# Performance work log

Measured on AMD Instinct MI355X. Metric: run time of the kernel, lower is better.

Reference implementation:

```python
import jax, jax.numpy as jnp
import numpy as np

HIDDEN = 2048
N_HEADS = 16
N_KV_HEADS = 4
HEAD_DIM = HIDDEN // N_HEADS  # 128
ROPE_THETA = 10000.0


def setup_inputs() -> dict:
    key = jax.random.key(0)
    ks = jax.random.split(key, 5)
    B, S = 2, 2048
    scale = 0.02
    return {
        "hidden_states": jax.random.normal(ks[0], (B, S, HIDDEN), jnp.float32),
        "Wq": jax.random.normal(ks[1], (HIDDEN, N_HEADS * HEAD_DIM), jnp.float32) * scale,
        "Wk": jax.random.normal(ks[2], (HIDDEN, N_KV_HEADS * HEAD_DIM), jnp.float32) * scale,
        "Wv": jax.random.normal(ks[3], (HIDDEN, N_KV_HEADS * HEAD_DIM), jnp.float32) * scale,
        "Wo": jax.random.normal(ks[4], (HIDDEN, HIDDEN), jnp.float32) * scale,
    }


def _rope_tables(seq_len, dim, dtype):
    inv_freq = 1.0 / (ROPE_THETA ** (jnp.arange(0, dim, 2, dtype=jnp.float32) / dim))
    t = jnp.arange(seq_len, dtype=jnp.float32)
    freqs = jnp.outer(t, inv_freq)            # [S, dim/2]
    emb = jnp.concatenate([freqs, freqs], -1)  # [S, dim]
    return jnp.cos(emb).astype(dtype), jnp.sin(emb).astype(dtype)


def _rotate_half(x):
    d = x.shape[-1] // 2
    return jnp.concatenate([-x[..., d:], x[..., :d]], axis=-1)


def _mqa_forward(hidden_states, Wq, Wk, Wv, Wo):
    B, S, _ = hidden_states.shape
    q = (hidden_states @ Wq).reshape(B, S, N_HEADS, HEAD_DIM).transpose(0, 2, 1, 3)      # [B,H,S,D]
    k = (hidden_states @ Wk).reshape(B, S, N_KV_HEADS, HEAD_DIM).transpose(0, 2, 1, 3)   # [B,Hkv,S,D]
    v = (hidden_states @ Wv).reshape(B, S, N_KV_HEADS, HEAD_DIM).transpose(0, 2, 1, 3)

    cos, sin = _rope_tables(S, HEAD_DIM, q.dtype)  # [S,D]
    q = q * cos + _rotate_half(q) * sin
    k = k * cos + _rotate_half(k) * sin

    # GQA: group query heads over shared KV heads instead of repeat_kv (same math)
    g = N_HEADS // N_KV_HEADS
    qg = q.reshape(B, N_KV_HEADS, g, S, HEAD_DIM)
    scale = 1.0 / np.sqrt(HEAD_DIM)
    scores = jnp.einsum("bhgqd,bhkd->bhgqk", qg, k) * scale  # [B,Hkv,g,S,S]
    causal = jnp.tril(jnp.ones((S, S), bool))
    scores = jnp.where(causal, scores, -jnp.inf)
    probs = jax.nn.softmax(scores.astype(jnp.float32), axis=-1).astype(q.dtype)
    out = jnp.einsum("bhgqk,bhkd->bhgqd", probs, v)  # [B,Hkv,g,S,D]
    out = out.reshape(B, N_HEADS, S, HEAD_DIM).transpose(0, 2, 1, 3).reshape(B, S, HIDDEN)
    return out @ Wo


def reference(hidden_states, Wq, Wk, Wv, Wo):
    return _mqa_forward(hidden_states, Wq, Wk, Wv, Wo)
```

## Files before the change

### kernel.cpp

```cpp
#include <hip/hip_runtime.h>
#include <hip/hip_bf16.h>
#include <cstdint>
#include <cstddef>

#define HIDDEN   2048
#define NH       16
#define NKV      4
#define HD       128
#define SEQ      2048
#define BATCH    2
#define NTOK     (BATCH*SEQ)
#define QKV_LD   3072
#define KOFF     2048
#define VOFF     2560
#define SM_SCALE 0.08838834764831845f
#define LOG2E    1.4426950408889634f

typedef __attribute__((ext_vector_type(8)))  short bf16x8;
typedef __attribute__((ext_vector_type(4)))  float f32x4v;
typedef __attribute__((ext_vector_type(16))) float f32x16;
typedef unsigned short ushort_t;

__device__ __forceinline__ unsigned short f2bf(float f) {
  return __builtin_bit_cast(unsigned short, __float2bfloat16(f));
}
__device__ __forceinline__ float bf2f(ushort_t u) {
  return __builtin_bit_cast(float, (unsigned)u << 16);
}
__device__ __forceinline__ unsigned pack2(float a, float b) {
  return (unsigned)f2bf(a) | ((unsigned)f2bf(b) << 16);
}

__device__ __forceinline__ void gload16(const void* g, void* l) {
  __builtin_amdgcn_global_load_lds(
      (const __attribute__((address_space(1))) unsigned int*)g,
      (__attribute__((address_space(3))) unsigned int*)l, 16, 0, 0);
}

__global__ __launch_bounds__(256) void conv_f2b(
    const float* __restrict__ in, ushort_t* __restrict__ out, int n8)
{
  const int i = blockIdx.x*256 + threadIdx.x;
  if (i >= n8) return;
  const float4 a = ((const float4*)in)[2*i];
  const float4 b = ((const float4*)in)[2*i + 1];
  uint4 r;
  r.x = pack2(a.x, a.y); r.y = pack2(a.z, a.w);
  r.z = pack2(b.x, b.y); r.w = pack2(b.z, b.w);
  ((uint4*)out)[i] = r;
}

__global__ __launch_bounds__(256) void transpose_f2b(
    const float* __restrict__ W, ushort_t* __restrict__ Wt, int K, int N)
{
  __shared__ float tile[32][33];
  const int n0 = blockIdx.x*32, k0 = blockIdx.y*32;
  const int tx = threadIdx.x & 31, ty = threadIdx.x >> 5;
  #pragma unroll
  for (int i = 0; i < 4; ++i)
    tile[ty*4 + i][tx] = W[(size_t)(k0 + ty*4 + i)*N + n0 + tx];
  __syncthreads();
  #pragma unroll
  for (int i = 0; i < 4; ++i) {
    const int nl = ty*4 + i;
    Wt[(size_t)(n0 + nl)*K + k0 + tx] = f2bf(tile[tx][nl]);
  }
}

template<bool B16OUT>
__global__ __launch_bounds__(256) void bt_gemm(
    const ushort_t* __restrict__ A, const ushort_t* __restrict__ Bt,
    void* __restrict__ Cv, int ldc)
{
  __shared__ ushort_t As[128*64];
  __shared__ ushort_t Bs[128*64];
  const int t = threadIdx.x, lane = t & 63, w = t >> 6;
  const int bm = blockIdx.y*128, bn = blockIdx.x*128;
  const int wr = w >> 1, wc = w & 1;
  const int lr = lane & 15, lg = lane >> 4;

  f32x4v acc[4][4];
  #pragma unroll
  for (int fm = 0; fm < 4; ++fm)
    #pragma unroll
    for (int fn = 0; fn < 4; ++fn)
      #pragma unroll
      for (int r = 0; r < 4; ++r) acc[fm][fn][r] = 0.f;

  const char* Ab = (const char*)A;
  const char* Bb = (const char*)Bt;
  char* asb = (char*)As;
  char* bsb = (char*)Bs;

  for (int kt = 0; kt < HIDDEN*2; kt += 128) {
    __syncthreads();
    #pragma unroll
    for (int u = 0; u < 4; ++u) {
      const int idx = u*256 + t;
      const int row = idx >> 3;
      const int kb  = (idx & 7) * 16;
      const int skb = kb ^ ((row & 7) << 4);
      gload16(Ab + (size_t)(bm + row)*4096 + kt + skb, asb + idx*16);
      gload16(Bb + (size_t)(bn + row)*4096 + kt + skb, bsb + idx*16);
    }
    __syncthreads();
    #pragma unroll
    for (int kc = 0; kc < 2; ++kc) {
      bf16x8 af[4], bfr[4];
      #pragma unroll
      for (int f = 0; f < 4; ++f) {
        const int rm = wr*64 + f*16 + lr;
        af[f]  = *(const bf16x8*)(asb + rm*128 + ((kc*64 + lg*16) ^ ((rm & 7) << 4)));
        const int rn = wc*64 + f*16 + lr;
        bfr[f] = *(const bf16x8*)(bsb + rn*128 + ((kc*64 + lg*16) ^ ((rn & 7) << 4)));
      }
      #pragma unroll
      for (int fm = 0; fm < 4; ++fm)
        #pragma unroll
        for (int fn = 0; fn < 4; ++fn)
          acc[fm][fn] = __builtin_amdgcn_mfma_f32_16x16x32_bf16(af[fm], bfr[fn], acc[fm][fn], 0, 0, 0);
    }
  }

  #pragma unroll
  for (int fm = 0; fm < 4; ++fm) {
    const int m = bm + wr*64 + fm*16 + lg*4;
    #pragma unroll
    for (int fn = 0; fn < 4; ++fn) {
      const int n = bn + wc*64 + fn*16 + lr;
      #pragma unroll
      for (int r = 0; r < 4; ++r) {
        if constexpr (B16OUT)
          ((ushort_t*)Cv)[(size_t)(m + r)*ldc + n] = f2bf(acc[fm][fn][r]);
        else
          ((float*)Cv)[(size_t)(m + r)*ldc + n] = acc[fm][fn][r];
      }
    }
  }
}

__global__ __launch_bounds__(256) void rope_conv(
    const ushort_t* __restrict__ QKVb, ushort_t* __restrict__ Qo,
    ushort_t* __restrict__ Ko)
{
  const int total = NTOK * (NH + NKV) * (HD/2);
  int idx = blockIdx.x * 256 + threadIdx.x;
  if (idx >= total) return;
  const int i   = idx & 63;
  int tmp = idx >> 6;
  const int hs  = tmp % (NH + NKV);
  const int tkn = tmp / (NH + NKV);
  const int s   = tkn & (SEQ - 1);
  const int b   = tkn >> 11;
  const float invf = expf(-(float)i * 0.14391156831212787f);
  float sn, cs;
  sincosf((float)s * invf, &sn, &cs);
  const size_t base = (size_t)tkn * QKV_LD + (hs < NH ? hs * HD : KOFF + (hs - NH) * HD);
  const float x0 = bf2f(QKVb[base + i]);
  const float x1 = bf2f(QKVb[base + i + 64]);
  const float y0 = x0 * cs - x1 * sn;
  const float y1 = x1 * cs + x0 * sn;
  if (hs < NH) {
    ushort_t* q = Qo + (size_t)tkn * HIDDEN + hs * HD;
    q[i]      = f2bf(y0 * (SM_SCALE * LOG2E));
    q[i + 64] = f2bf(y1 * (SM_SCALE * LOG2E));
  } else {
    ushort_t* k = Ko + ((size_t)(b*NKV + (hs - NH))*SEQ + s) * HD;
    k[i]      = f2bf(y0);
    k[i + 64] = f2bf(y1);
  }
}

__global__ __launch_bounds__(256) void vt_conv(
    const ushort_t* __restrict__ QKVb, ushort_t* __restrict__ Vtb)
{
  __shared__ ushort_t tile[32][33];
  const int s0 = blockIdx.x*32;
  const int d0 = (blockIdx.y & 3)*32;
  const int bk = blockIdx.y >> 2;
  const int b = bk >> 2, hk = bk & 3;
  const int tx = threadIdx.x & 31, ty = threadIdx.x >> 5;
  #pragma unroll
  for (int i = 0; i < 4; ++i) {
    const int sl = ty*4 + i;
    tile[sl][tx] = QKVb[(size_t)(b*SEQ + s0 + sl)*QKV_LD + VOFF + hk*HD + d0 + tx];
  }
  __syncthreads();
  #pragma unroll
  for (int i = 0; i < 4; ++i) {
    const int dl = ty*4 + i;
    Vtb[((size_t)bk*HD + d0 + dl)*SEQ + s0 + tx] = tile[tx][dl];
  }
}

__global__ __launch_bounds__(128) void attn_mfma4(
    const ushort_t* __restrict__ Qb, const ushort_t* __restrict__ Kb,
    const ushort_t* __restrict__ Vtb, ushort_t* __restrict__ O)
{
  __shared__ ushort_t Kl[64*128];
  __shared__ ushort_t Vl[128*64];
  __shared__ ushort_t Pl[2][32*64];

  const int bh = blockIdx.x;
  const int qb = 31 - blockIdx.y;
  const int b = bh >> 4, h = bh & 15, hk = h >> 2;
  const int t = threadIdx.x, w = t >> 6, lane = t & 63;
  const int c = lane & 31, hi = lane >> 5;
  const int qw0 = qb*64 + w*32;
  const int qg  = qw0 + c;

  const char* Kbb = (const char*)(Kb + (size_t)(b*NKV + hk)*SEQ*HD);
  const char* Vbb = (const char*)(Vtb + (size_t)(b*NKV + hk)*HD*SEQ);
  char* plb = (char*)Pl[w];
  char* klds = (char*)Kl;
  char* vlds = (char*)Vl;

  int ksrc[8], vsrc[8], ldst[8];
  #pragma unroll
  for (int u = 0; u < 8; ++u) {
    const int idx = u*128 + t;
    const int krow = idx >> 4, kof = (idx & 15) << 4;
    ksrc[u] = krow*256 + (kof ^ ((krow & 15) << 4));
    const int vd = idx >> 3,  vof = (idx & 7) << 4;
    vsrc[u] = vd*(SEQ*2) + (vof ^ ((vd & 7) << 4));
    ldst[u] = idx*16;
  }

  bf16x8 qf[8];
  {
    const ushort_t* qrow = Qb + (size_t)(b*SEQ + qg)*HIDDEN + h*HD;
    #pragma unroll
    for (int kc = 0; kc < 8; ++kc)
      qf[kc] = *(const bf16x8*)(qrow + kc*16 + hi*8);
  }

  f32x16 ot[4];
  #pragma unroll
  for (int nc = 0; nc < 4; ++nc)
    #pragma unroll
    for (int r = 0; r < 16; ++r) ot[nc][r] = 0.f;
  float m = -1e30f, l = 0.f;

  #pragma unroll
  for (int u = 0; u < 8; ++u) {
    gload16(Kbb + ksrc[u], klds + ldst[u]);
    gload16(Vbb + vsrc[u], vlds + ldst[u]);
  }
  __syncthreads();

  for (int kt = 0; kt <= qb; ++kt) {
    f32x16 s[2];
    #pragma unroll
    for (int kn = 0; kn < 2; ++kn)
      #pragma unroll
      for (int r = 0; r < 16; ++r) s[kn][r] = 0.f;
    #pragma unroll
    for (int kn = 0; kn < 2; ++kn) {
      const int row = kn*32 + c;
      const int sw = (row & 15) << 4;
      #pragma unroll
      for (int kc = 0; kc < 8; ++kc) {
        const bf16x8 ka = *(const bf16x8*)(klds + row*256 + ((kc*32 + hi*16) ^ sw));
        s[kn] = __builtin_amdgcn_mfma_f32_32x32x16_bf16(ka, qf[kc], s[kn], 0, 0, 0);
      }
    }
    if (kt == qb) {
      #pragma unroll
      for (int kn = 0; kn < 2; ++kn)
        #pragma unroll
        for (int r = 0; r < 16; ++r) {
          const int kg_ = kt*64 + kn*32 + (r & 3) + 8*(r >> 2) + 4*hi;
          if (kg_ > qg) s[kn][r] = -1e30f;
        }
    }
    float mx[16];
    #pragma unroll
    for (int r = 0; r < 16; ++r) mx[r] = fmaxf(s[0][r], s[1][r]);
    #pragma unroll
    for (int st = 8; st > 0; st >>= 1)
      #pragma unroll
      for (int r = 0; r < 8; ++r)
        if (r < st) mx[r] = fmaxf(mx[r], mx[r + st]);
    const float pm = fmaxf(mx[0], __shfl_xor(mx[0], 32));
    if (!__all(pm - m <= 8.f)) {
      const float mnew = fmaxf(m, pm);
      const float corr = exp2f(m - mnew);
      m = mnew;
      l *= corr;
      #pragma unroll
      for (int nc = 0; nc < 4; ++nc) ot[nc] *= corr;
    }
    float ls = 0.f;
    #pragma unroll
    for (int kn = 0; kn < 2; ++kn)
      #pragma unroll
      for (int r = 0; r < 16; ++r) {
        const float p = exp2f(s[kn][r] - m);
        ls += p;
        s[kn][r] = p;
      }
    l += ls;
    {
      const int swp = (c & 7) << 4;
      #pragma unroll
      for (int kn = 0; kn < 2; ++kn)
        #pragma unroll
        for (int r = 0; r < 16; r += 2) {
          const int key = kn*32 + (r & 3) + 8*(r >> 2) + 4*hi;
          *(unsigned*)(plb + c*128 + ((key*2) ^ swp)) = pack2(s[kn][r], s[kn][r+1]);
        }
    }
    asm volatile("s_waitcnt lgkmcnt(0)" ::: "memory");
    #pragma unroll
    for (int kc = 0; kc < 4; ++kc) {
      const bf16x8 pb = *(const bf16x8*)(plb + c*128 + ((kc*32 + hi*16) ^ ((c & 7) << 4)));
      #pragma unroll
      for (int nc = 0; nc < 4; ++nc) {
        const int dim = nc*32 + c;
        const bf16x8 va = *(const bf16x8*)(vlds + dim*128 + ((kc*32 + hi*16) ^ ((dim & 7) << 4)));
        ot[nc] = __builtin_amdgcn_mfma_f32_32x32x16_bf16(va, pb, ot[nc], 0, 0, 0);
      }
    }
    if (kt < qb) {
      __syncthreads();
      const size_t kto = (size_t)(kt + 1) * 16384;
      const int    vto = (kt + 1) * 128;
      #pragma unroll
      for (int u = 0; u < 8; ++u) {
        gload16(Kbb + kto + ksrc[u], klds + ldst[u]);
        gload16(Vbb + vto + vsrc[u], vlds + ldst[u]);
      }
      __syncthreads();
    }
  }

  const float lt = l + __shfl_xor(l, 32);
  const float inv = 1.f / lt;
  ushort_t* orow = O + (size_t)(b*SEQ + qg) * HIDDEN + h*HD;
  #pragma unroll
  for (int nc = 0; nc < 4; ++nc)
    #pragma unroll
    for (int r = 0; r < 16; r += 2) {
      const int dim = nc*32 + (r & 3) + 8*(r >> 2) + 4*hi;
      *(unsigned*)(orow + dim) = pack2(ot[nc][r]*inv, ot[nc][r+1]*inv);
    }
}

extern "C" void kernel_launch(void* const* d_in, const int* in_sizes, int n_in,
                              void* d_out, int out_size, void* d_ws, size_t ws_size,
                              hipStream_t stream)
{
  (void)in_sizes; (void)n_in; (void)out_size; (void)ws_size;
  const float* H  = (const float*)d_in[0];
  const float* Wq = (const float*)d_in[1];
  const float* Wk = (const float*)d_in[2];
  const float* Wv = (const float*)d_in[3];
  const float* Wo = (const float*)d_in[4];
  float* out = (float*)d_out;

  char* ws = (char*)d_ws;
  ushort_t* QKVb = (ushort_t*)ws;
  ushort_t* Hb   = (ushort_t*)(ws + 25165824);
  ushort_t* Qb   = Hb;
  ushort_t* Wt   = (ushort_t*)(ws + 41943040);
  ushort_t* Kb   = (ushort_t*)(ws + 54525952);
  ushort_t* Vtb  = (ushort_t*)(ws + 58720256);
  ushort_t* Oat  = (ushort_t*)(ws + 62914560);

  conv_f2b<<<4096, 256, 0, stream>>>(H, Hb, NTOK*HIDDEN/8);
  transpose_f2b<<<dim3(64, 64), 256, 0, stream>>>(Wq, Wt,                     2048, 2048);
  transpose_f2b<<<dim3(16, 64), 256, 0, stream>>>(Wk, Wt + (size_t)2048*2048, 2048, 512);
  transpose_f2b<<<dim3(16, 64), 256, 0, stream>>>(Wv, Wt + (size_t)2560*2048, 2048, 512);

  bt_gemm<true><<<dim3(QKV_LD/128, NTOK/128), 256, 0, stream>>>(Hb, Wt, QKVb, QKV_LD);

  const int rope_total = NTOK * (NH + NKV) * (HD/2);
  rope_conv<<<(rope_total + 255)/256, 256, 0, stream>>>(QKVb, Qb, Kb);
  vt_conv<<<dim3(SEQ/32, 32), 256, 0, stream>>>(QKVb, Vtb);

  attn_mfma4<<<dim3(32, 32), 128, 0, stream>>>(Qb, Kb, Vtb, Oat);

  transpose_f2b<<<dim3(64, 64), 256, 0, stream>>>(Wo, Wt, 2048, 2048);
  bt_gemm<false><<<dim3(HIDDEN/128, NTOK/128), 256, 0, stream>>>(Oat, Wt, out, HIDDEN);
}
```

Baseline: 244.2 us.

## Split attention KV range across four waves per 32-query tile with LDS merge

The attention kernel changes from two waves each owning 32 queries over a 64-key tile to four waves sharing one 32-query tile. Each wave handles a different 32-key slice of a 128-key K/V tile, and the per-wave softmax states are merged at the end through shared memory. This doubles the grid and uses larger K/V tiles, aiming for more parallelism and fewer barriers per key. The cost is 80KB of LDS per block, which limits occupancy, plus an extra reduction pass and idle waves on the diagonal tiles.

```diff
diff --git a/kernel.cpp b/kernel.cpp
--- a/kernel.cpp
+++ b/kernel.cpp
@@ -193,37 +193,32 @@
   }
 }
 
-__global__ __launch_bounds__(128) void attn_mfma4(
+__global__ __launch_bounds__(256) void attn_mfma5(
     const ushort_t* __restrict__ Qb, const ushort_t* __restrict__ Kb,
     const ushort_t* __restrict__ Vtb, ushort_t* __restrict__ O)
 {
-  __shared__ ushort_t Kl[64*128];
-  __shared__ ushort_t Vl[128*64];
-  __shared__ ushort_t Pl[2][32*64];
+  __shared__ char smem[81920];
 
   const int bh = blockIdx.x;
-  const int qb = 31 - blockIdx.y;
+  const int qt = 63 - (int)blockIdx.y;
   const int b = bh >> 4, h = bh & 15, hk = h >> 2;
   const int t = threadIdx.x, w = t >> 6, lane = t & 63;
   const int c = lane & 31, hi = lane >> 5;
-  const int qw0 = qb*64 + w*32;
+  const int qw0 = qt*32;
   const int qg  = qw0 + c;
+  const int nsteps = (qt + 4) >> 2;
 
   const char* Kbb = (const char*)(Kb + (size_t)(b*NKV + hk)*SEQ*HD);
   const char* Vbb = (const char*)(Vtb + (size_t)(b*NKV + hk)*HD*SEQ);
-  char* plb = (char*)Pl[w];
-  char* klds = (char*)Kl;
-  char* vlds = (char*)Vl;
-
-  int ksrc[8], vsrc[8], ldst[8];
+  char* plb = smem + 65536 + w*4096;
+
+  int ksrc[8], vsrc[8];
   #pragma unroll
   for (int u = 0; u < 8; ++u) {
-    const int idx = u*128 + t;
-    const int krow = idx >> 4, kof = (idx & 15) << 4;
-    ksrc[u] = krow*256 + (kof ^ ((krow & 15) << 4));
-    const int vd = idx >> 3,  vof = (idx & 7) << 4;
-    vsrc[u] = vd*(SEQ*2) + (vof ^ ((vd & 7) << 4));
-    ldst[u] = idx*16;
+    const int idx = u*256 + t;
+    const int row = idx >> 4, of = (idx & 15) << 4;
+    ksrc[u] = row*256 + (of ^ ((row & 15) << 4));
+    vsrc[u] = row*(SEQ*2) + (of ^ ((row & 15) << 4));
   }
 
   bf16x8 qf[8];
@@ -239,111 +234,137 @@
   for (int nc = 0; nc < 4; ++nc)
     #pragma unroll
     for (int r = 0; r < 16; ++r) ot[nc][r] = 0.f;
-  float m = -1e30f, l = 0.f;
+  float m = -3000.f, l = 0.f;
 
   #pragma unroll
   for (int u = 0; u < 8; ++u) {
-    gload16(Kbb + ksrc[u], klds + ldst[u]);
-    gload16(Vbb + vsrc[u], vlds + ldst[u]);
+    const int idx = u*256 + t;
+    gload16(Kbb + ksrc[u], smem + idx*16);
+    gload16(Vbb + vsrc[u], smem + 32768 + idx*16);
   }
   __syncthreads();
 
-  for (int kt = 0; kt <= qb; ++kt) {
-    f32x16 s[2];
-    #pragma unroll
-    for (int kn = 0; kn < 2; ++kn)
-      #pragma unroll
-      for (int r = 0; r < 16; ++r) s[kn][r] = 0.f;
-    #pragma unroll
-    for (int kn = 0; kn < 2; ++kn) {
-      const int row = kn*32 + c;
-      const int sw = (row & 15) << 4;
-      #pragma unroll
-      for (int kc = 0; kc < 8; ++kc) {
-        const bf16x8 ka = *(const bf16x8*)(klds + row*256 + ((kc*32 + hi*16) ^ sw));
-        s[kn] = __builtin_amdgcn_mfma_f32_32x32x16_bf16(ka, qf[kc], s[kn], 0, 0, 0);
-      }
-    }
-    if (kt == qb) {
-      #pragma unroll
-      for (int kn = 0; kn < 2; ++kn)
+  for (int ktp = 0; ktp < nsteps; ++ktp) {
+    const bool skip = (ktp*128 + w*32) > (qw0 + 31);
+    if (!skip) {
+      f32x16 s;
+      #pragma unroll
+      for (int r = 0; r < 16; ++r) s[r] = 0.f;
+      {
+        const int key = w*32 + c;
+        const int sw = (key & 15) << 4;
+        const char* krow = smem + key*256;
+        #pragma unroll
+        for (int kc = 0; kc < 8; ++kc) {
+          const bf16x8 ka = *(const bf16x8*)(krow + ((kc*32 + hi*16) ^ sw));
+          s = __builtin_amdgcn_mfma_f32_32x32x16_bf16(ka, qf[kc], s, 0, 0, 0);
+        }
+      }
+      if (ktp*128 + 127 > qw0) {
         #pragma unroll
         for (int r = 0; r < 16; ++r) {
-          const int kg_ = kt*64 + kn*32 + (r & 3) + 8*(r >> 2) + 4*hi;
-          if (kg_ > qg) s[kn][r] = -1e30f;
+          const int kg_ = ktp*128 + w*32 + (r & 3) + 8*(r >> 2) + 4*hi;
+          if (kg_ > qg) s[r] = -30000.f;
         }
-    }
-    float mx[16];
-    #pragma unroll
-    for (int r = 0; r < 16; ++r) mx[r] = fmaxf(s[0][r], s[1][r]);
-    #pragma unroll
-    for (int st = 8; st > 0; st >>= 1)
-      #pragma unroll
-      for (int r = 0; r < 8; ++r)
-        if (r < st) mx[r] = fmaxf(mx[r], mx[r + st]);
-    const float pm = fmaxf(mx[0], __shfl_xor(mx[0], 32));
-    if (!__all(pm - m <= 8.f)) {
-      const float mnew = fmaxf(m, pm);
-      const float corr = exp2f(m - mnew);
-      m = mnew;
-      l *= corr;
-      #pragma unroll
-      for (int nc = 0; nc < 4; ++nc) ot[nc] *= corr;
-    }
-    float ls = 0.f;
-    #pragma unroll
-    for (int kn = 0; kn < 2; ++kn)
+      }
+      float mx[8];
+      #pragma unroll
+      for (int r = 0; r < 8; ++r) mx[r] = fmaxf(s[r], s[r + 8]);
+      #pragma unroll
+      for (int st = 4; st > 0; st >>= 1)
+        #pragma unroll
+        for (int r = 0; r < 4; ++r)
+          if (r < st) mx[r] = fmaxf(mx[r], mx[r + st]);
+      const float pm = fmaxf(mx[0], __shfl_xor(mx[0], 32));
+      if (!__all(pm - m <= 8.f)) {
+        const float mnew = fmaxf(m, pm);
+        const float corr = exp2f(m - mnew);
+        m = mnew;
+        l *= corr;
+        #pragma unroll
+        for (int nc = 0; nc < 4; ++nc) ot[nc] *= corr;
+      }
+      float ls = 0.f;
       #pragma unroll
       for (int r = 0; r < 16; ++r) {
-        const float p = exp2f(s[kn][r] - m);
+        const float p = exp2f(s[r] - m);
         ls += p;
-        s[kn][r] = p;
-      }
-    l += ls;
-    {
-      const int swp = (c & 7) << 4;
-      #pragma unroll
-      for (int kn = 0; kn < 2; ++kn)
+        s[r] = p;
+      }
+      l += ls;
+      {
+        const int swp = (c & 7) << 4;
         #pragma unroll
         for (int r = 0; r < 16; r += 2) {
-          const int key = kn*32 + (r & 3) + 8*(r >> 2) + 4*hi;
-          *(unsigned*)(plb + c*128 + ((key*2) ^ swp)) = pack2(s[kn][r], s[kn][r+1]);
+          const int kl_ = (r & 3) + 8*(r >> 2) + 4*hi;
+          *(unsigned*)(plb + c*128 + ((kl_*2) ^ swp)) = pack2(s[r], s[r+1]);
         }
-    }
-    asm volatile("s_waitcnt lgkmcnt(0)" ::: "memory");
-    #pragma unroll
-    for (int kc = 0; kc < 4; ++kc) {
-      const bf16x8 pb = *(const bf16x8*)(plb + c*128 + ((kc*32 + hi*16) ^ ((c & 7) << 4)));
-      #pragma unroll
-      for (int nc = 0; nc < 4; ++nc) {
-        const int dim = nc*32 + c;
-        const bf16x8 va = *(const bf16x8*)(vlds + dim*128 + ((kc*32 + hi*16) ^ ((dim & 7) << 4)));
-        ot[nc] = __builtin_amdgcn_mfma_f32_32x32x16_bf16(va, pb, ot[nc], 0, 0, 0);
-      }
-    }
-    if (kt < qb) {
+      }
+      asm volatile("s_waitcnt lgkmcnt(0)" ::: "memory");
+      #pragma unroll
+      for (int kcl = 0; kcl < 2; ++kcl) {
+        const bf16x8 pb = *(const bf16x8*)(plb + c*128 + ((kcl*32 + hi*16) ^ ((c & 7) << 4)));
+        #pragma unroll
+        for (int nc = 0; nc < 4; ++nc) {
+          const int dim = nc*32 + c;
+          const bf16x8 va = *(const bf16x8*)(smem + 32768 + dim*256 +
+              ((w*64 + kcl*32 + hi*16) ^ ((dim & 15) << 4)));
+          ot[nc] = __builtin_amdgcn_mfma_f32_32x32x16_bf16(va, pb, ot[nc], 0, 0, 0);
+        }
+      }
+    }
+    if (ktp < nsteps - 1) {
       __syncthreads();
-      const size_t kto = (size_t)(kt + 1) * 16384;
-      const int    vto = (kt + 1) * 128;
+      const size_t kto = (size_t)(ktp + 1) * 32768;
+      const int    vto = (ktp + 1) * 256;
       #pragma unroll
       for (int u = 0; u < 8; ++u) {
-        gload16(Kbb + kto + ksrc[u], klds + ldst[u]);
-        gload16(Vbb + vto + vsrc[u], vlds + ldst[u]);
+        const int idx = u*256 + t;
+        gload16(Kbb + kto + ksrc[u], smem + idx*16);
+        gload16(Vbb + vto + vsrc[u], smem + 32768 + idx*16);
       }
       __syncthreads();
     }
   }
 
-  const float lt = l + __shfl_xor(l, 32);
-  const float inv = 1.f / lt;
-  ushort_t* orow = O + (size_t)(b*SEQ + qg) * HIDDEN + h*HD;
-  #pragma unroll
-  for (int nc = 0; nc < 4; ++nc)
-    #pragma unroll
-    for (int r = 0; r < 16; r += 2) {
-      const int dim = nc*32 + (r & 3) + 8*(r >> 2) + 4*hi;
-      *(unsigned*)(orow + dim) = pack2(ot[nc][r]*inv, ot[nc][r+1]*inv);
-    }
+  __syncthreads();
+  float* ob = (float*)smem;
+  if (w > 0) {
+    float* dst = ob + ((w - 1)*64 + lane)*66;
+    #pragma unroll
+    for (int nc = 0; nc < 4; ++nc)
+      #pragma unroll
+      for (int r = 0; r < 16; ++r) dst[nc*16 + r] = ot[nc][r];
+    dst[64] = m;
+    dst[65] = l;
+  }
+  __syncthreads();
+  if (w == 0) {
+    #pragma unroll 1
+    for (int wi = 0; wi < 3; ++wi) {
+      const float* src = ob + (wi*64 + lane)*66;
+      const float mw = src[64], lw = src[65];
+      const float mn = fmaxf(m, mw);
+      const float c0 = exp2f(m - mn), c1 = exp2f(mw - mn);
+      m = mn;
+      l = l*c0 + lw*c1;
+      #pragma unroll
+      for (int nc = 0; nc < 4; ++nc)
+        #pragma unroll
+        for (int r = 0; r < 16; ++r)
+          ot[nc][r] = ot[nc][r]*c0 + src[nc*16 + r]*c1;
+    }
+    const float lt = l + __shfl_xor(l, 32);
+    const float inv = 1.f / lt;
+    ushort_t* orow = O + (size_t)(b*SEQ + qg) * HIDDEN + h*HD;
+    #pragma unroll
+    for (int nc = 0; nc < 4; ++nc)
+      #pragma unroll
+      for (int r = 0; r < 16; r += 2) {
+        const int dim = nc*32 + (r & 3) + 8*(r >> 2) + 4*hi;
+        *(unsigned*)(orow + dim) = pack2(ot[nc][r]*inv, ot[nc][r+1]*inv);
+      }
+  }
 }
 
 extern "C" void kernel_launch(void* const* d_in, const int* in_sizes, int n_in,
@@ -378,7 +399,7 @@
   rope_conv<<<(rope_total + 255)/256, 256, 0, stream>>>(QKVb, Qb, Kb);
   vt_conv<<<dim3(SEQ/32, 32), 256, 0, stream>>>(QKVb, Vtb);
 
-  attn_mfma4<<<dim3(32, 32), 128, 0, stream>>>(Qb, Kb, Vtb, Oat);
+  attn_mfma5<<<dim3(32, 64), 256, 0, stream>>>(Qb, Kb, Vtb, Oat);
 
   transpose_f2b<<<dim3(64, 64), 256, 0, stream>>>(Wo, Wt, 2048, 2048);
   bt_gemm<false><<<dim3(HIDDEN/128, NTOK/128), 256, 0, stream>>>(Oat, Wt, out, HIDDEN);
```

Result: slower. 324.3 us (+32.8%).
